# Optimization experiments

Hardware: AMD Instinct MI355X
Metric: run time of the kernel (lower is better)

The kernel has to match this reference:

```python
import jax, jax.numpy as jnp
import numpy as np

B, DIN, DK, DV, H, DOUT = 16384, 2048, 2048, 2048, 16, 512
dk, dv = DK // H, DV // H  # 128, 128

def setup_inputs() -> dict:
    key = jax.random.key(0)
    ks = jax.random.split(key, 10)
    s_in = 1.0 / np.sqrt(DIN)
    s_v = 1.0 / np.sqrt(DV)
    s_2in = 1.0 / np.sqrt(2 * DIN)
    return {
        "x": jax.random.normal(ks[0], (B, DIN), jnp.float32),
        "Wq": jax.random.normal(ks[1], (DIN, DK), jnp.float32) * s_in,
        "Wk": jax.random.normal(ks[2], (DIN, DK), jnp.float32) * s_in,
        "Wv": jax.random.normal(ks[3], (DIN, DV), jnp.float32) * s_in,
        "Wo": jax.random.normal(ks[4], (DV, DIN), jnp.float32) * s_v,
        "bo": jax.random.normal(ks[5], (DIN,), jnp.float32) * s_v,
        "Wg": jax.random.normal(ks[6], (2 * DIN, DIN), jnp.float32) * s_2in,
        "bg": jax.random.normal(ks[7], (DIN,), jnp.float32) * s_2in,
        "Wout": jax.random.normal(ks[8], (DIN, DOUT), jnp.float32) * s_in,
        "bout": jax.random.normal(ks[9], (DOUT,), jnp.float32) * s_in,
    }

def _feat(t):
    # kernel feature map: relu(x) + 1e-4
    return jax.nn.relu(t) + 1e-4

def reference(x, Wq, Wk, Wv, Wo, bo, Wg, bg, Wout, bout):
    b = x.shape[0]
    q = _feat((x @ Wq).reshape(b, H, dk))
    k = _feat((x @ Wk).reshape(b, H, dk))
    v = (x @ Wv).reshape(b, H, dv)
    # linear attention: aggregate over batch (acts as sequence)
    kv = jnp.einsum('bhd,bhe->hde', k, v)            # [H, dk, dv]
    z = 1.0 / (jnp.einsum('bhd,hd->bh', q, k.sum(axis=0)) + 1e-6)  # [B, H]
    att = jnp.einsum('bhd,hde->bhe', q, kv) * z[..., None]         # [B, H, dv]
    att = att.reshape(b, DV)
    out_proj = att @ Wo + bo
    gate = jax.nn.sigmoid(jnp.concatenate([out_proj, x], axis=-1) @ Wg + bg)
    out = gate * out_proj + (1.0 - gate) * x
    return out @ Wout + bout
```

## Files before the change

kernel.cpp:

```cpp
#include <hip/hip_runtime.h>
#include <hip/hip_bf16.h>
#include <math.h>

typedef __bf16 bf16_t;
typedef __attribute__((ext_vector_type(8))) __bf16 bf16x8;
typedef __attribute__((ext_vector_type(4))) __bf16 bf16x4;
typedef __attribute__((ext_vector_type(16))) float f32x16;

#define DEVI __device__ __forceinline__

constexpr int B_SZ = 16384, DIN = 2048, DK = 2048, DV = 2048, NH = 16, DOUT = 512;

DEVI void load_lds16(const void* gptr, void* lptr) {
  __builtin_amdgcn_global_load_lds(
      (const __attribute__((address_space(1))) unsigned int*)gptr,
      (__attribute__((address_space(3))) unsigned int*)lptr,
      16, 0, 0);
}

template <int EPI>
__global__ __launch_bounds__(512, 2) void gemm256(
    const bf16_t* __restrict__ A, int lda, long aZ,
    const bf16_t* __restrict__ Bt, int ldb, long bZ,
    void* __restrict__ Cv, int ldc, long cZ, int K,
    const float* __restrict__ aux1,
    const float* __restrict__ aux2) {
  __shared__ __align__(16) bf16_t lds[2][2][256 * 64];
  const int tid = threadIdx.x;
  const int gx = gridDim.x;
  const int nwg = gx * gridDim.y;
  int flat = blockIdx.y * gx + blockIdx.x;
  flat = (flat & 7) * (nwg >> 3) + (flat >> 3);
  const int bn = flat % gx, bm = flat / gx;
  const int bz = blockIdx.z;

  const int lane = tid & 63, w = tid >> 6;
  const int wr = w >> 2, wc = w & 3;
  const int lm = lane & 31, lh = lane >> 5;

  const bf16_t* __restrict__ Ab = A + (long)bm * 256 * lda + (long)bz * aZ;
  const bf16_t* __restrict__ Bb = Bt + (long)bn * 256 * ldb + (long)bz * bZ;

  const int srow = tid >> 3;
  const int fs = (srow & 7) ^ ((srow >> 3) & 3);
  const int sslot = (tid & 7) ^ fs;
  const long aOff = (long)srow * lda + sslot * 8;
  const long bOff = (long)srow * ldb + sslot * 8;
  char* const ldsc = (char*)&lds[0][0][0];

  const int xorv = (lm & 7) ^ ((lm >> 3) & 3);
  const int rbA = (wr * 128 + lm) * 128;
  const int rbB = (wc * 64 + lm) * 128 + 32768;
  int sl16[4];
#pragma unroll
  for (int s = 0; s < 4; ++s) sl16[s] = (((2 * s) | lh) ^ xorv) * 16;

  auto stageA = [&](int buf, int t, int h) {
    const bf16_t* p = Ab + aOff + t * 64 + (long)h * 128 * lda;
    char* d = ldsc + buf * 65536 + h * 16384 + tid * 16;
    load_lds16(p, d);
    load_lds16(p + (long)64 * lda, d + 8192);
  };
  auto stageB = [&](int buf, int t, int h) {
    const bf16_t* p = Bb + bOff + t * 64 + (long)h * 128 * ldb;
    char* d = ldsc + buf * 65536 + 32768 + h * 16384 + tid * 16;
    load_lds16(p, d);
    load_lds16(p + (long)64 * ldb, d + 8192);
  };

  f32x16 acc[4][2] = {};
  const int NT = K >> 6;

  stageA(0, 0, 0); stageA(0, 0, 1); stageB(0, 0, 0); stageB(0, 0, 1);
  if (NT > 1) {
    stageB(1, 1, 0); stageB(1, 1, 1);
    asm volatile("s_waitcnt vmcnt(4)" ::: "memory");
  } else {
    asm volatile("s_waitcnt vmcnt(0)" ::: "memory");
  }
  __builtin_amdgcn_sched_barrier(0);
  __builtin_amdgcn_s_barrier();

  for (int t = 0; t < NT; ++t) {
    const int cur = t & 1;
    const char* base = ldsc + cur * 65536;
    bf16x8 af[2][4], bq[2][4];
#pragma unroll
    for (int s = 0; s < 4; ++s)
      af[0][s] = *(const bf16x8*)(base + rbA + 0 * 4096 + sl16[s]);
#pragma unroll
    for (int j = 0; j < 2; ++j)
#pragma unroll
      for (int s = 0; s < 4; ++s)
        bq[j][s] = *(const bf16x8*)(base + rbB + j * 4096 + sl16[s]);
#pragma unroll
    for (int s = 0; s < 4; ++s)
      af[1][s] = *(const bf16x8*)(base + rbA + 1 * 4096 + sl16[s]);
    if (t + 1 < NT) { stageA(cur ^ 1, t + 1, 0); stageA(cur ^ 1, t + 1, 1); }
    __builtin_amdgcn_s_setprio(1);
#pragma unroll
    for (int s = 0; s < 4; ++s) {
      acc[0][0] = __builtin_amdgcn_mfma_f32_32x32x16_bf16(af[0][s], bq[0][s], acc[0][0], 0, 0, 0);
      acc[0][1] = __builtin_amdgcn_mfma_f32_32x32x16_bf16(af[0][s], bq[1][s], acc[0][1], 0, 0, 0);
      acc[1][0] = __builtin_amdgcn_mfma_f32_32x32x16_bf16(af[1][s], bq[0][s], acc[1][0], 0, 0, 0);
      acc[1][1] = __builtin_amdgcn_mfma_f32_32x32x16_bf16(af[1][s], bq[1][s], acc[1][1], 0, 0, 0);
    }
    __builtin_amdgcn_s_setprio(0);
    asm volatile("s_waitcnt lgkmcnt(0)" ::: "memory");
    __builtin_amdgcn_sched_barrier(0);
    __builtin_amdgcn_s_barrier();
#pragma unroll
    for (int s = 0; s < 4; ++s)
      af[0][s] = *(const bf16x8*)(base + rbA + 2 * 4096 + sl16[s]);
#pragma unroll
    for (int s = 0; s < 4; ++s)
      af[1][s] = *(const bf16x8*)(base + rbA + 3 * 4096 + sl16[s]);
    if (t + 2 < NT) { stageB(cur, t + 2, 0); stageB(cur, t + 2, 1); }
    __builtin_amdgcn_s_setprio(1);
#pragma unroll
    for (int s = 0; s < 4; ++s) {
      acc[2][0] = __builtin_amdgcn_mfma_f32_32x32x16_bf16(af[0][s], bq[0][s], acc[2][0], 0, 0, 0);
      acc[2][1] = __builtin_amdgcn_mfma_f32_32x32x16_bf16(af[0][s], bq[1][s], acc[2][1], 0, 0, 0);
      acc[3][0] = __builtin_amdgcn_mfma_f32_32x32x16_bf16(af[1][s], bq[0][s], acc[3][0], 0, 0, 0);
      acc[3][1] = __builtin_amdgcn_mfma_f32_32x32x16_bf16(af[1][s], bq[1][s], acc[3][1], 0, 0, 0);
    }
    __builtin_amdgcn_s_setprio(0);
    if (t + 2 < NT) asm volatile("s_waitcnt vmcnt(4) lgkmcnt(0)" ::: "memory");
    else            asm volatile("s_waitcnt vmcnt(0) lgkmcnt(0)" ::: "memory");
    __builtin_amdgcn_sched_barrier(0);
    __builtin_amdgcn_s_barrier();
  }

#pragma unroll
  for (int i = 0; i < 4; ++i) {
#pragma unroll
    for (int j = 0; j < 2; ++j) {
      const int col = bn * 256 + wc * 64 + j * 32 + lm;
#pragma unroll
      for (int r = 0; r < 16; ++r) {
        const int row = bm * 256 + wr * 128 + i * 32 + (r & 3) + 8 * (r >> 2) + 4 * lh;
        const long cidx = (long)row * ldc + (long)bz * cZ + col;
        float val = acc[i][j][r];
        if (EPI == 0) {
          ((bf16_t*)Cv)[cidx] = (bf16_t)val;
        } else if (EPI == 1) {
          if (col < 4096) val = fmaxf(val, 0.f) + 1e-4f;
          ((bf16_t*)Cv)[cidx] = (bf16_t)val;
        } else if (EPI == 2) {
          val += aux1[col];
          ((bf16_t*)Cv)[cidx] = (bf16_t)val;
        } else if (EPI == 4) {
          const float g = 1.f / (1.f + __expf(-(val + aux1[col])));
          const float op = (float)A[(long)row * lda + col];
          const float xx = aux2[(long)row * DIN + col];
          ((bf16_t*)Cv)[cidx] = (bf16_t)(g * op + (1.f - g) * xx);
        } else if (EPI == 5) {
          ((float*)Cv)[cidx] = val + aux1[col];
        }
      }
    }
  }
}

template <int EPI>
__global__ __launch_bounds__(256, 4) void gemm_bt(
    const bf16_t* __restrict__ A, int lda, long aZ,
    const bf16_t* __restrict__ Bt, int ldb, long bZ,
    void* __restrict__ Cv, int ldc, long cZ, int K,
    const float* __restrict__ aux1,
    const float* __restrict__ aux2) {
  __shared__ __align__(16) bf16_t As[2][128 * 32];
  __shared__ __align__(16) bf16_t Bs[2][128 * 32];
  const int tid = threadIdx.x;
  const int bn = blockIdx.x, bm = blockIdx.y, bz = blockIdx.z;
  const int lane = tid & 63, w = tid >> 6;
  const int wm = (w & 1) * 64, wn = (w >> 1) * 64;
  const int lm = lane & 31, lh = lane >> 5;

  const bf16_t* __restrict__ Ab = A + (long)bm * 128 * lda + (long)bz * aZ;
  const bf16_t* __restrict__ Bb = Bt + (long)bn * 128 * ldb + (long)bz * bZ;

  const int srow = tid >> 2, scol = (tid & 3) * 8;
  const long aRow = (long)srow * lda + scol;
  const long bRow = (long)srow * ldb + scol;

  const char* aBase = (const char*)As + (wm + lm) * 64 + lh * 16;
  const char* bBase = (const char*)Bs + (wn + lm) * 64 + lh * 16;

  f32x16 acc[2][2] = {};

  for (int k0 = 0; k0 < K; k0 += 64) {
    const bf16_t* ap = Ab + aRow + k0;
    const bf16_t* bp = Bb + bRow + k0;
    load_lds16(ap, &As[0][tid * 8]);
    load_lds16(ap + (long)64 * lda, &As[0][2048 + tid * 8]);
    load_lds16(ap + 32, &As[1][tid * 8]);
    load_lds16(ap + (long)64 * lda + 32, &As[1][2048 + tid * 8]);
    load_lds16(bp, &Bs[0][tid * 8]);
    load_lds16(bp + (long)64 * ldb, &Bs[0][2048 + tid * 8]);
    load_lds16(bp + 32, &Bs[1][tid * 8]);
    load_lds16(bp + (long)64 * ldb + 32, &Bs[1][2048 + tid * 8]);
    __syncthreads();
#pragma unroll
    for (int s = 0; s < 4; ++s) {
      const int off = (s >> 1) * 8192 + (s & 1) * 32;
      const bf16x8 af0 = *(const bf16x8*)(aBase + off);
      const bf16x8 af1 = *(const bf16x8*)(aBase + off + 2048);
      const bf16x8 bf0 = *(const bf16x8*)(bBase + off);
      const bf16x8 bf1 = *(const bf16x8*)(bBase + off + 2048);
      acc[0][0] = __builtin_amdgcn_mfma_f32_32x32x16_bf16(af0, bf0, acc[0][0], 0, 0, 0);
      acc[0][1] = __builtin_amdgcn_mfma_f32_32x32x16_bf16(af0, bf1, acc[0][1], 0, 0, 0);
      acc[1][0] = __builtin_amdgcn_mfma_f32_32x32x16_bf16(af1, bf0, acc[1][0], 0, 0, 0);
      acc[1][1] = __builtin_amdgcn_mfma_f32_32x32x16_bf16(af1, bf1, acc[1][1], 0, 0, 0);
    }
    __syncthreads();
  }

#pragma unroll
  for (int i = 0; i < 2; ++i) {
#pragma unroll
    for (int j = 0; j < 2; ++j) {
      const int col = bn * 128 + wn + j * 32 + lm;
#pragma unroll
      for (int r = 0; r < 16; ++r) {
        const int row = bm * 128 + wm + i * 32 + (r & 3) + 8 * (r >> 2) + 4 * lh;
        const long cidx = (long)row * ldc + (long)bz * cZ + col;
        float val = acc[i][j][r];
        if (EPI == 0) {
          ((bf16_t*)Cv)[cidx] = (bf16_t)val;
        } else if (EPI == 5) {
          ((float*)Cv)[cidx] = val + aux1[col];
        }
      }
    }
  }
}

__global__ __launch_bounds__(256) void prep_kernel(
    const float* __restrict__ x, const float* __restrict__ Wq,
    const float* __restrict__ Wk, const float* __restrict__ Wv,
    const float* __restrict__ Wo, const float* __restrict__ Wg,
    const float* __restrict__ Wout, bf16_t* __restrict__ concat,
    bf16_t* __restrict__ WqkvT, bf16_t* __restrict__ WoT,
    bf16_t* __restrict__ WgT, bf16_t* __restrict__ WoutT) {
  const int tid = threadIdx.x;
  int b = blockIdx.x;
  if (b < 32768) {
    const long i = ((long)b * 256 + tid) * 4;
    const long row = i >> 11;
    const int col = (int)(i & 2047);
    const float4 f = *(const float4*)&x[i];
    bf16x4 o;
    o[0] = (bf16_t)f.x; o[1] = (bf16_t)f.y; o[2] = (bf16_t)f.z; o[3] = (bf16_t)f.w;
    *(bf16x4*)&concat[row * 4096 + 2048 + col] = o;
    return;
  }
  b -= 32768;
  const float* in; bf16_t* out; int R, C;
  if (b < 4096)       { in = Wq;   out = WqkvT;                     R = 2048; C = 2048; }
  else if (b < 8192)  { in = Wk;   out = WqkvT + (size_t)2048*2048; R = 2048; C = 2048; b -= 4096; }
  else if (b < 12288) { in = Wv;   out = WqkvT + (size_t)4096*2048; R = 2048; C = 2048; b -= 8192; }
  else if (b < 16384) { in = Wo;   out = WoT;                       R = 2048; C = 2048; b -= 12288; }
  else if (b < 24576) { in = Wg;   out = WgT;                       R = 4096; C = 2048; b -= 16384; }
  else                { in = Wout; out = WoutT;                     R = 2048; C = 512;  b -= 24576; }
  const int CB = C / 32;
  const int c0 = (b % CB) * 32, r0 = (b / CB) * 32;
  __shared__ bf16_t tile[32][33];
  const int tx = tid & 31, ty = tid >> 5;
  for (int i = ty; i < 32; i += 8)
    tile[i][tx] = (bf16_t)in[(long)(r0 + i) * C + c0 + tx];
  __syncthreads();
  for (int i = ty; i < 32; i += 8)
    out[(long)(c0 + i) * R + r0 + tx] = tile[tx][i];
}

__global__ __launch_bounds__(256) void ksum_kernel(const bf16_t* __restrict__ qkv,
                                                   float* __restrict__ ksum) {
  const int col = blockIdx.x * 256 + threadIdx.x;
  const int r0 = blockIdx.y * 256;
  const bf16_t* k = qkv + 2048;
  float s = 0.f;
  for (int r = 0; r < 256; ++r) s += (float)k[(long)(r0 + r) * 6144 + col];
  atomicAdd(&ksum[col], s);
}

__global__ __launch_bounds__(256) void kv_kernel(const bf16_t* __restrict__ qkv,
                                                 float* __restrict__ P) {
  const int h = blockIdx.x, sp = blockIdx.y;
  const int t = threadIdx.x;
  __shared__ __align__(16) bf16_t kS[64 * 128];
  __shared__ __align__(16) bf16_t vS[64 * 128];
  const int d0 = (t >> 4) * 8, e0 = (t & 15) * 8;
  const int srow = t >> 4, scol = (t & 15) * 8;
  float acc[8][8] = {};
  const bf16_t* kp = qkv + 2048 + h * 128;
  const bf16_t* vp = qkv + 4096 + h * 128;
  const long base = (long)sp * 512 * 6144;
  for (int c0 = 0; c0 < 512; c0 += 64) {
#pragma unroll
    for (int it = 0; it < 4; ++it) {
      load_lds16(kp + base + (long)(c0 + it * 16 + srow) * 6144 + scol, &kS[it * 2048 + t * 8]);
      load_lds16(vp + base + (long)(c0 + it * 16 + srow) * 6144 + scol, &vS[it * 2048 + t * 8]);
    }
    __syncthreads();
    for (int bb = 0; bb < 64; ++bb) {
      const bf16x8 kk = *(const bf16x8*)&kS[bb * 128 + d0];
      const bf16x8 vv = *(const bf16x8*)&vS[bb * 128 + e0];
      float kf[8], vf[8];
#pragma unroll
      for (int r = 0; r < 8; ++r) { kf[r] = (float)kk[r]; vf[r] = (float)vv[r]; }
#pragma unroll
      for (int a = 0; a < 8; ++a)
#pragma unroll
        for (int b2 = 0; b2 < 8; ++b2) acc[a][b2] += kf[a] * vf[b2];
    }
    __syncthreads();
  }
  float* Ph = P + (long)h * 16384;
#pragma unroll
  for (int a = 0; a < 8; ++a)
#pragma unroll
    for (int b2 = 0; b2 < 8; ++b2)
      atomicAdd(&Ph[(d0 + a) * 128 + e0 + b2], acc[a][b2]);
}

__global__ __launch_bounds__(256) void cvt_bf(const float* __restrict__ P,
                                              bf16_t* __restrict__ o, int n) {
  const int i = blockIdx.x * 256 + threadIdx.x;
  if (i < n) o[i] = (bf16_t)P[i];
}

__global__ __launch_bounds__(256) void z_kernel(bf16_t* __restrict__ qkv,
                                                const float* __restrict__ ksum) {
  __shared__ float ks[2048];
  const int t = threadIdx.x;
  for (int i = t; i < 2048; i += 256) ks[i] = ksum[i];
  __syncthreads();
  const int b = blockIdx.x * 16 + (t >> 4);
  const int h = t & 15;
  bf16_t* qr = qkv + (long)b * 6144 + h * 128;
  bf16x8 qq[16];
  float s = 0.f;
#pragma unroll
  for (int i = 0; i < 16; ++i) {
    qq[i] = *(const bf16x8*)&qr[i * 8];
#pragma unroll
    for (int r = 0; r < 8; ++r) s += (float)qq[i][r] * ks[h * 128 + i * 8 + r];
  }
  const float z = 1.f / (s + 1e-6f);
#pragma unroll
  for (int i = 0; i < 16; ++i) {
#pragma unroll
    for (int r = 0; r < 8; ++r) qq[i][r] = (bf16_t)((float)qq[i][r] * z);
    *(bf16x8*)&qr[i * 8] = qq[i];
  }
}

extern "C" void kernel_launch(void* const* d_in, const int* in_sizes, int n_in,
                              void* d_out, int out_size, void* d_ws, size_t ws_size,
                              hipStream_t stream) {
  const float* x    = (const float*)d_in[0];
  const float* Wq   = (const float*)d_in[1];
  const float* Wk   = (const float*)d_in[2];
  const float* Wv   = (const float*)d_in[3];
  const float* Wo   = (const float*)d_in[4];
  const float* bo   = (const float*)d_in[5];
  const float* Wg   = (const float*)d_in[6];
  const float* bg   = (const float*)d_in[7];
  const float* Wout = (const float*)d_in[8];
  const float* bout = (const float*)d_in[9];

  char* ws = (char*)d_ws;
  size_t off = 0;
  auto alloc = [&](size_t bytes) -> void* {
    void* p = ws + off;
    off += (bytes + 255) & ~(size_t)255;
    return p;
  };
  bf16_t* concat = (bf16_t*)alloc((size_t)B_SZ * 4096 * 2);
  bf16_t* qkv    = (bf16_t*)alloc((size_t)B_SZ * 6144 * 2);
  bf16_t* outb   = (bf16_t*)alloc((size_t)B_SZ * DIN * 2);
  bf16_t* WqkvT  = (bf16_t*)alloc((size_t)6144 * DIN * 2);
  bf16_t* WoT    = (bf16_t*)alloc((size_t)DIN * DV * 2);
  bf16_t* WgT    = (bf16_t*)alloc((size_t)DIN * 4096 * 2);
  bf16_t* WoutT  = (bf16_t*)alloc((size_t)DOUT * DIN * 2);
  float*  P      = (float*)alloc((size_t)NH * 128 * 128 * 4);
  bf16_t* kvbf   = (bf16_t*)alloc((size_t)NH * 128 * 128 * 2);
  bf16_t* G      = (bf16_t*)alloc((size_t)DIN * DK * 2);
  float*  ksum   = (float*)alloc((size_t)DK * 4);

  hipMemsetAsync(P, 0, (size_t)NH * 128 * 128 * 4, stream);
  hipMemsetAsync(ksum, 0, (size_t)DK * 4, stream);

  prep_kernel<<<32768 + 25600, 256, 0, stream>>>(x, Wq, Wk, Wv, Wo, Wg, Wout,
                                                 concat, WqkvT, WoT, WgT, WoutT);

  const bf16_t* xb = concat + 2048;

  gemm256<1><<<dim3(24, 64, 1), 512, 0, stream>>>(xb, 4096, 0, WqkvT, 2048, 0,
                                                  qkv, 6144, 0, 2048, nullptr, nullptr);

  ksum_kernel<<<dim3(8, 64), 256, 0, stream>>>(qkv, ksum);
  kv_kernel<<<dim3(16, 32), 256, 0, stream>>>(qkv, P);
  cvt_bf<<<1024, 256, 0, stream>>>(P, kvbf, NH * 128 * 128);
  z_kernel<<<B_SZ / 16, 256, 0, stream>>>(qkv, ksum);

  gemm_bt<0><<<dim3(1, 16, 16), 256, 0, stream>>>(WoT, 2048, 128, kvbf, 128, 16384,
                                                  G, 2048, 128, 128, nullptr, nullptr);

  gemm256<2><<<dim3(8, 64, 1), 512, 0, stream>>>(qkv, 6144, 0, G, 2048, 0,
                                                 concat, 4096, 0, 2048, bo, nullptr);

  gemm256<4><<<dim3(8, 64, 1), 512, 0, stream>>>(concat, 4096, 0, WgT, 4096, 0,
                                                 outb, 2048, 0, 4096, bg, x);

  gemm_bt<5><<<dim3(4, 128, 1), 256, 0, stream>>>(outb, 2048, 0, WoutT, 2048, 0,
                                                  d_out, 512, 0, 2048, bout, nullptr);
}
```

Measured before the change: 1.522 ms.

## Issue all A-fragment LDS reads up front and overlap with staged MFMA groups

Each K-tile now reads all four A row-fragments from LDS at the start, instead of reading two, computing, syncing and reading two more. MFMA work is split into four groups gated by partial lgkmcnt waits, so each group can start once its own fragments have landed. The mid-tile barrier moves earlier, ahead of the B prefetch for tile t+2. This raises register pressure (16 A fragments live at once) and relies on LDS loads and hand-counted waits completing in the expected order.

```diff
diff --git a/kernel.cpp b/kernel.cpp
--- a/kernel.cpp
+++ b/kernel.cpp
@@ -84,49 +84,69 @@
   for (int t = 0; t < NT; ++t) {
     const int cur = t & 1;
     const char* base = ldsc + cur * 65536;
-    bf16x8 af[2][4], bq[2][4];
+    bf16x8 a0[4], a1[4], a2[4], a3[4], bq[2][4];
 #pragma unroll
     for (int s = 0; s < 4; ++s)
-      af[0][s] = *(const bf16x8*)(base + rbA + 0 * 4096 + sl16[s]);
+      a0[s] = *(const bf16x8*)(base + rbA + 0 * 4096 + sl16[s]);
 #pragma unroll
     for (int j = 0; j < 2; ++j)
 #pragma unroll
       for (int s = 0; s < 4; ++s)
         bq[j][s] = *(const bf16x8*)(base + rbB + j * 4096 + sl16[s]);
+    __builtin_amdgcn_sched_barrier(0);
 #pragma unroll
     for (int s = 0; s < 4; ++s)
-      af[1][s] = *(const bf16x8*)(base + rbA + 1 * 4096 + sl16[s]);
+      a1[s] = *(const bf16x8*)(base + rbA + 1 * 4096 + sl16[s]);
+    __builtin_amdgcn_sched_barrier(0);
+#pragma unroll
+    for (int s = 0; s < 4; ++s)
+      a2[s] = *(const bf16x8*)(base + rbA + 2 * 4096 + sl16[s]);
+    __builtin_amdgcn_sched_barrier(0);
+#pragma unroll
+    for (int s = 0; s < 4; ++s)
+      a3[s] = *(const bf16x8*)(base + rbA + 3 * 4096 + sl16[s]);
+    __builtin_amdgcn_sched_barrier(0);
     if (t + 1 < NT) { stageA(cur ^ 1, t + 1, 0); stageA(cur ^ 1, t + 1, 1); }
+    asm volatile("s_waitcnt lgkmcnt(12)" ::: "memory");
+    __builtin_amdgcn_sched_barrier(0);
     __builtin_amdgcn_s_setprio(1);
 #pragma unroll
     for (int s = 0; s < 4; ++s) {
-      acc[0][0] = __builtin_amdgcn_mfma_f32_32x32x16_bf16(af[0][s], bq[0][s], acc[0][0], 0, 0, 0);
-      acc[0][1] = __builtin_amdgcn_mfma_f32_32x32x16_bf16(af[0][s], bq[1][s], acc[0][1], 0, 0, 0);
-      acc[1][0] = __builtin_amdgcn_mfma_f32_32x32x16_bf16(af[1][s], bq[0][s], acc[1][0], 0, 0, 0);
-      acc[1][1] = __builtin_amdgcn_mfma_f32_32x32x16_bf16(af[1][s], bq[1][s], acc[1][1], 0, 0, 0);
+      acc[0][0] = __builtin_amdgcn_mfma_f32_32x32x16_bf16(a0[s], bq[0][s], acc[0][0], 0, 0, 0);
+      acc[0][1] = __builtin_amdgcn_mfma_f32_32x32x16_bf16(a0[s], bq[1][s], acc[0][1], 0, 0, 0);
+    }
+    __builtin_amdgcn_s_setprio(0);
+    asm volatile("s_waitcnt lgkmcnt(8)" ::: "memory");
+    __builtin_amdgcn_sched_barrier(0);
+    __builtin_amdgcn_s_setprio(1);
+#pragma unroll
+    for (int s = 0; s < 4; ++s) {
+      acc[1][0] = __builtin_amdgcn_mfma_f32_32x32x16_bf16(a1[s], bq[0][s], acc[1][0], 0, 0, 0);
+      acc[1][1] = __builtin_amdgcn_mfma_f32_32x32x16_bf16(a1[s], bq[1][s], acc[1][1], 0, 0, 0);
+    }
+    __builtin_amdgcn_s_setprio(0);
+    __builtin_amdgcn_s_barrier();
+    if (t + 2 < NT) { stageB(cur, t + 2, 0); stageB(cur, t + 2, 1); }
+    asm volatile("s_waitcnt lgkmcnt(4)" ::: "memory");
+    __builtin_amdgcn_sched_barrier(0);
+    __builtin_amdgcn_s_setprio(1);
+#pragma unroll
+    for (int s = 0; s < 4; ++s) {
+      acc[2][0] = __builtin_amdgcn_mfma_f32_32x32x16_bf16(a2[s], bq[0][s], acc[2][0], 0, 0, 0);
+      acc[2][1] = __builtin_amdgcn_mfma_f32_32x32x16_bf16(a2[s], bq[1][s], acc[2][1], 0, 0, 0);
     }
     __builtin_amdgcn_s_setprio(0);
     asm volatile("s_waitcnt lgkmcnt(0)" ::: "memory");
     __builtin_amdgcn_sched_barrier(0);
-    __builtin_amdgcn_s_barrier();
-#pragma unroll
-    for (int s = 0; s < 4; ++s)
-      af[0][s] = *(const bf16x8*)(base + rbA + 2 * 4096 + sl16[s]);
-#pragma unroll
-    for (int s = 0; s < 4; ++s)
-      af[1][s] = *(const bf16x8*)(base + rbA + 3 * 4096 + sl16[s]);
-    if (t + 2 < NT) { stageB(cur, t + 2, 0); stageB(cur, t + 2, 1); }
     __builtin_amdgcn_s_setprio(1);
 #pragma unroll
     for (int s = 0; s < 4; ++s) {
-      acc[2][0] = __builtin_amdgcn_mfma_f32_32x32x16_bf16(af[0][s], bq[0][s], acc[2][0], 0, 0, 0);
-      acc[2][1] = __builtin_amdgcn_mfma_f32_32x32x16_bf16(af[0][s], bq[1][s], acc[2][1], 0, 0, 0);
-      acc[3][0] = __builtin_amdgcn_mfma_f32_32x32x16_bf16(af[1][s], bq[0][s], acc[3][0], 0, 0, 0);
-      acc[3][1] = __builtin_amdgcn_mfma_f32_32x32x16_bf16(af[1][s], bq[1][s], acc[3][1], 0, 0, 0);
+      acc[3][0] = __builtin_amdgcn_mfma_f32_32x32x16_bf16(a3[s], bq[0][s], acc[3][0], 0, 0, 0);
+      acc[3][1] = __builtin_amdgcn_mfma_f32_32x32x16_bf16(a3[s], bq[1][s], acc[3][1], 0, 0, 0);
     }
     __builtin_amdgcn_s_setprio(0);
-    if (t + 2 < NT) asm volatile("s_waitcnt vmcnt(4) lgkmcnt(0)" ::: "memory");
-    else            asm volatile("s_waitcnt vmcnt(0) lgkmcnt(0)" ::: "memory");
+    if (t + 2 < NT) asm volatile("s_waitcnt vmcnt(4)" ::: "memory");
+    else            asm volatile("s_waitcnt vmcnt(0)" ::: "memory");
     __builtin_amdgcn_sched_barrier(0);
     __builtin_amdgcn_s_barrier();
   }
```

Measured after the change: 1.491 ms. 1.02x faster.
